# Kernel tuning notes

Hardware: AMD Instinct MI355X
Metric: run time of the kernel (lower is better)

Reference implementation:

```python
import jax, jax.numpy as jnp
import numpy as np

R, M, T = 512, 64, 128
D0, DL, D1, DE = 100, 100, 1000, 100  # embed_dim0, lstm_dim, hidden, embed_dim


def setup_inputs() -> dict:
    key = jax.random.key(0)
    ks = jax.random.split(key, 16)
    s = 0.05
    return {
        "routes": jax.random.normal(ks[0], (R, M, T, 3), dtype=jnp.float32),
        "W0": jax.random.normal(ks[1], (D0, 3), dtype=jnp.float32) * s,
        "b0": jnp.zeros((D0,), dtype=jnp.float32),
        "W_ih": jax.random.normal(ks[2], (4 * DL, D0), dtype=jnp.float32) * s,
        "b_ih": jnp.zeros((4 * DL,), dtype=jnp.float32),
        "W_hh": jax.random.normal(ks[3], (4 * DL, DL), dtype=jnp.float32) * s,
        "b_hh": jnp.zeros((4 * DL,), dtype=jnp.float32),
        "W1": jax.random.normal(ks[4], (D1, DL), dtype=jnp.float32) * s,
        "b1": jnp.zeros((D1,), dtype=jnp.float32),
        "W2": jax.random.normal(ks[5], (DE, D1), dtype=jnp.float32) * s,
        "b2": jnp.zeros((DE,), dtype=jnp.float32),
        "h0": jax.random.uniform(ks[6], (1, DL), dtype=jnp.float32),
        "c0": jax.random.uniform(ks[7], (1, DL), dtype=jnp.float32),
    }


def _forward(routes, W0, b0, W_ih, b_ih, W_hh, b_hh, W1, b1, W2, b2, h0, c0):
    # In the original, LSTMCell is re-run from (h0,c0) at every timestep and hx is
    # overwritten, so only the LAST point of each route matters mathematically.
    last = routes[:, :, -1, :].reshape(-1, 3)           # [R*M, 3]
    x = last @ W0.T + b0                                 # linear0 -> [R*M, D0]
    gates = x @ W_ih.T + b_ih + (h0 @ W_hh.T + b_hh)     # one LSTMCell step, [R*M, 4*DL]
    i, f, g, o = jnp.split(gates, 4, axis=-1)            # PyTorch gate order i,f,g,o
    c = jax.nn.sigmoid(f) * c0 + jax.nn.sigmoid(i) * jnp.tanh(g)
    h = jax.nn.sigmoid(o) * jnp.tanh(c)                  # [R*M, DL]
    h = jax.nn.relu(h @ W1.T + b1) @ W2.T + b2           # MLP -> [R*M, DE]
    emb = h.reshape(R, M, DE).sum(axis=1)                # sum-pool routes -> [R, DE]
    emb = emb / jnp.linalg.norm(emb, axis=-1, keepdims=True)
    cov = emb @ emb.T                                    # cosine similarity [R, R]
    idx = jnp.arange(R)
    return cov.at[idx, idx].set(-jnp.inf)


def reference(routes, W0, b0, W_ih, b_ih, W_hh, b_hh, W1, b1, W2, b2, h0, c0):
    return _forward(routes, W0, b0, W_ih, b_ih, W_hh, b_hh, W1, b1, W2, b2, h0, c0)
```

## Files before the change

kernel.cpp:

```cpp
#include <hip/hip_runtime.h>
#include <hip/hip_bf16.h>
#include <math.h>
#include <float.h>

#define R_ 512
#define M_ 64
#define T_ 128
#define D0_ 100
#define DL_ 100
#define D1_ 1000
#define DE_ 100

#define DIAG_SENTINEL (-1.0e38f)

typedef __attribute__((ext_vector_type(8))) short bf16x8;
typedef __attribute__((ext_vector_type(4))) float f32x4;

__device__ __forceinline__ float sigmoidf_(float x){
  return __builtin_amdgcn_rcpf(1.0f + __expf(-x));
}
__device__ __forceinline__ float tanhf_(float x){
  return 1.0f - 2.0f*__builtin_amdgcn_rcpf(__expf(2.0f*x) + 1.0f);
}
__device__ __forceinline__ short f2bf(float x){
  unsigned u = __builtin_bit_cast(unsigned, x);
  u = (u + 0x7fffu + ((u >> 16) & 1u)) >> 16;
  return (short)u;
}

__global__ __launch_bounds__(256) void k_setup(const float* __restrict__ W1,
                          short* __restrict__ W1pack,
                          const float* __restrict__ W0, const float* __restrict__ b0,
                          const float* __restrict__ W_ih, const float* __restrict__ b_ih,
                          const float* __restrict__ W_hh, const float* __restrict__ b_hh,
                          const float* __restrict__ h0,
                          float* __restrict__ Wc, float* __restrict__ bc) {
  int b = blockIdx.x;
  int tid = threadIdx.x;
  if (b < 64){
    int t = b*256 + tid;
    int l = t & 63, ks = (t>>6)&3, ntile = t>>8;
    int n  = ntile*16 + (l&15);
    int j0 = ks*32 + ((l>>4)<<3);
    bf16x8 v;
    #pragma unroll
    for (int u=0;u<8;++u){
      int j = j0 + u;
      float x = (n < D1_ && j < DL_) ? W1[n*DL_ + j] : 0.f;
      v[u] = f2bf(x);
    }
    ((bf16x8*)W1pack)[t] = v;
  } else {
    int j = (b-64)*256 + tid;
    if (j >= 4*DL_) return;
    float a0=0.f,a1=0.f,a2=0.f,ab=0.f,ah=0.f;
    for (int k=0;k<D0_;++k){
      float w = W_ih[j*D0_+k];
      a0 += w*W0[k*3+0]; a1 += w*W0[k*3+1]; a2 += w*W0[k*3+2];
      ab += w*b0[k];
    }
    for (int k=0;k<DL_;++k) ah += W_hh[j*DL_+k]*h0[k];
    Wc[j*3+0]=a0; Wc[j*3+1]=a1; Wc[j*3+2]=a2;
    bc[j] = ab + b_ih[j] + ah + b_hh[j];
  }
}

__global__ __launch_bounds__(512, 4) void k_fused(const float* __restrict__ routes,
                       const float* __restrict__ Wc, const float* __restrict__ bc,
                       const float* __restrict__ c0,
                       const short* __restrict__ W1pack,
                       const float* __restrict__ b1,
                       const float* __restrict__ W2, const float* __restrict__ b2,
                       float* __restrict__ embT) {
  __shared__ __align__(16) short Hl[8192];
  __shared__ __align__(16) float ts[1000];
  __shared__ float WcS[1200];
  __shared__ float bcS[400];
  __shared__ float c0S[100];
  __shared__ float b1S[1000];
  int r = blockIdx.x;
  int tid = threadIdx.x;
  int w = tid >> 6, l = tid & 63, lr = l & 15;

  float lx[2][3];
  #pragma unroll
  for (int h=0;h<2;++h){
    int mw = h*8 + w;
    int m = mw >> 2;
    int row = r*64 + m*16 + lr;
    const float* lp = routes + ((size_t)row*T_ + (T_-1))*3;
    lx[h][0] = lp[0]; lx[h][1] = lp[1]; lx[h][2] = lp[2];
  }
  for (int i=tid; i<1200; i+=512) WcS[i] = Wc[i];
  for (int i=tid; i<400;  i+=512) bcS[i] = bc[i];
  for (int i=tid; i<100;  i+=512) c0S[i] = c0[i];
  for (int i=tid; i<1000; i+=512) b1S[i] = b1[i];
  __syncthreads();

  {
    int ks = w & 3;
    int j0 = ks*32 + ((l>>4)<<3);
    #pragma unroll
    for (int h=0;h<2;++h){
      int mw = h*8 + w;
      float l0 = lx[h][0], l1 = lx[h][1], l2 = lx[h][2];
      bf16x8 v;
      #pragma unroll
      for (int u=0;u<8;++u){
        int j = j0 + u;
        float hh = 0.f;
        if (j < DL_){
          int ji = j, jf = 100+j, jg = 200+j, jo = 300+j;
          float gi = bcS[ji] + l0*WcS[ji*3+0] + l1*WcS[ji*3+1] + l2*WcS[ji*3+2];
          float gf = bcS[jf] + l0*WcS[jf*3+0] + l1*WcS[jf*3+1] + l2*WcS[jf*3+2];
          float gg = bcS[jg] + l0*WcS[jg*3+0] + l1*WcS[jg*3+1] + l2*WcS[jg*3+2];
          float go = bcS[jo] + l0*WcS[jo*3+0] + l1*WcS[jo*3+1] + l2*WcS[jo*3+2];
          float cc = sigmoidf_(gf)*c0S[j] + sigmoidf_(gi)*tanhf_(gg);
          hh = sigmoidf_(go)*tanhf_(cc);
        }
        v[u] = f2bf(hh);
      }
      *(bf16x8*)&Hl[(mw*64 + l)*8] = v;
    }
  }
  __syncthreads();

  bf16x8 a[4][4];
  #pragma unroll
  for (int m=0;m<4;++m)
    #pragma unroll
    for (int ks=0;ks<4;++ks)
      a[m][ks] = *(const bf16x8*)&Hl[((m*4+ks)*64 + l)*8];

  const bf16x8* Wp = (const bf16x8*)W1pack;
  #pragma unroll 2
  for (int q=0;q<8;++q){
    int ntile = w*8 + q;
    if (ntile == 63) continue;
    f32x4 acc[4];
    #pragma unroll
    for (int m=0;m<4;++m) acc[m] = (f32x4){0.f,0.f,0.f,0.f};
    #pragma unroll
    for (int ks=0;ks<4;++ks){
      bf16x8 bfrag = Wp[(ntile*4+ks)*64 + l];
      #pragma unroll
      for (int m=0;m<4;++m)
        acc[m] = __builtin_amdgcn_mfma_f32_16x16x32_bf16(a[m][ks], bfrag, acc[m], 0, 0, 0);
    }
    int n = ntile*16 + lr;
    float b1n = (n < D1_) ? b1S[n] : 0.f;
    float s = 0.f;
    #pragma unroll
    for (int m=0;m<4;++m){
      #pragma unroll
      for (int jj=0;jj<4;++jj) s += fmaxf(acc[m][jj] + b1n, 0.f);
    }
    s += __shfl_xor(s, 16);
    s += __shfl_xor(s, 32);
    if (l < 16 && n < D1_) ts[n] = s;
  }
  __syncthreads();

  int g = tid >> 2, el = tid & 3;
  if (g < DE_){
    const float4* wrow = (const float4*)(W2 + (size_t)g*D1_);
    const float4* trow = (const float4*)ts;
    float acc = 0.f;
    #pragma unroll 8
    for (int k4 = el; k4 < 250; k4 += 4){
      float4 wv = wrow[k4], tv = trow[k4];
      acc += wv.x*tv.x + wv.y*tv.y + wv.z*tv.z + wv.w*tv.w;
    }
    acc += __shfl_xor(acc, 1);
    acc += __shfl_xor(acc, 2);
    if (el == 0) embT[(size_t)g*R_ + r] = acc + 64.f*b2[g];
  }
}

__global__ __launch_bounds__(256) void k_cov(const float* __restrict__ embT,
                                             float* __restrict__ out) {
  __shared__ float a[2][100];
  int i0 = blockIdx.x * 2, tid = threadIdx.x;
  if (tid < 200){
    int ii = tid & 1, k = tid >> 1;
    a[ii][k] = embT[(size_t)k*R_ + i0 + ii];
  }
  __syncthreads();
  int j = tid, j2 = tid + 256;
  float acc[2] = {0.f,0.f}, acc2[2] = {0.f,0.f};
  float ssi[2] = {0.f,0.f};
  float ssj = 0.f, ssj2 = 0.f;
  #pragma unroll 4
  for (int k=0;k<100;++k){
    float x = embT[(size_t)k*R_ + j];
    float y = embT[(size_t)k*R_ + j2];
    ssj += x*x; ssj2 += y*y;
    #pragma unroll
    for (int ii=0;ii<2;++ii){
      float av = a[ii][k];
      acc[ii]  += av*x;
      acc2[ii] += av*y;
      ssi[ii]  += av*av;
    }
  }
  float rnj  = rsqrtf(ssj);
  float rnj2 = rsqrtf(ssj2);
  #pragma unroll
  for (int ii=0;ii<2;++ii){
    int i = i0 + ii;
    float rni = rsqrtf(ssi[ii]);
    out[(size_t)i*R_ + j]  = (j  == i) ? DIAG_SENTINEL : acc[ii]*rni*rnj;
    out[(size_t)i*R_ + j2] = (j2 == i) ? DIAG_SENTINEL : acc2[ii]*rni*rnj2;
  }
}

extern "C" void kernel_launch(void* const* d_in, const int* in_sizes, int n_in,
                              void* d_out, int out_size, void* d_ws, size_t ws_size,
                              hipStream_t stream) {
  const float* routes = (const float*)d_in[0];
  const float* W0   = (const float*)d_in[1];
  const float* b0   = (const float*)d_in[2];
  const float* W_ih = (const float*)d_in[3];
  const float* b_ih = (const float*)d_in[4];
  const float* W_hh = (const float*)d_in[5];
  const float* b_hh = (const float*)d_in[6];
  const float* W1   = (const float*)d_in[7];
  const float* b1   = (const float*)d_in[8];
  const float* W2   = (const float*)d_in[9];
  const float* b2   = (const float*)d_in[10];
  const float* h0   = (const float*)d_in[11];
  const float* c0   = (const float*)d_in[12];
  float* out = (float*)d_out;

  char* ws = (char*)d_ws;
  short* W1pack = (short*)(ws);
  float* Wc     = (float*)(ws + 262144);
  float* bc     = (float*)(ws + 262144 + 4800);
  float* embT   = (float*)(ws + 268544);

  hipLaunchKernelGGL(k_setup, dim3(66), dim3(256), 0, stream,
                     W1, W1pack, W0,b0,W_ih,b_ih,W_hh,b_hh,h0, Wc, bc);
  hipLaunchKernelGGL(k_fused, dim3(512), dim3(512), 0, stream,
                     routes, Wc, bc, c0, W1pack, b1, W2, b2, embT);
  hipLaunchKernelGGL(k_cov, dim3(256), dim3(256), 0, stream,
                     embT, out);
}
```

Before: 43.05 us.

## Split fused MLP across two blocks per route and batch W2 in separate kernel

The fused kernel now uses two blocks per route, each computing half of the W1 output tiles and writing the pooled hidden sums to global memory. A new k_emb kernel applies W2 for four routes per block, reusing each W2 row across them. The setup kernel's gate-precompute now uses 16 threads per output row with shuffle reductions instead of one serial thread per row. This trades extra global traffic for the intermediate sums and one more kernel launch against more parallelism, higher occupancy, and less per-block serial W2 work.

Result: slower. 104.4 us (+142.4%).

```diff
diff --git a/kernel.cpp b/kernel.cpp
--- a/kernel.cpp
+++ b/kernel.cpp
@@ -51,34 +51,40 @@
     }
     ((bf16x8*)W1pack)[t] = v;
   } else {
-    int j = (b-64)*256 + tid;
-    if (j >= 4*DL_) return;
+    int j = (b-64)*16 + (tid >> 4);
+    int kl = tid & 15;
     float a0=0.f,a1=0.f,a2=0.f,ab=0.f,ah=0.f;
-    for (int k=0;k<D0_;++k){
-      float w = W_ih[j*D0_+k];
+    for (int k = kl; k < D0_; k += 16){
+      float w = W_ih[j*D0_ + k];
       a0 += w*W0[k*3+0]; a1 += w*W0[k*3+1]; a2 += w*W0[k*3+2];
       ab += w*b0[k];
-    }
-    for (int k=0;k<DL_;++k) ah += W_hh[j*DL_+k]*h0[k];
-    Wc[j*3+0]=a0; Wc[j*3+1]=a1; Wc[j*3+2]=a2;
-    bc[j] = ab + b_ih[j] + ah + b_hh[j];
-  }
-}
-
-__global__ __launch_bounds__(512, 4) void k_fused(const float* __restrict__ routes,
+      ah += W_hh[j*DL_ + k]*h0[k];
+    }
+    #pragma unroll
+    for (int m=1;m<16;m<<=1){
+      a0 += __shfl_xor(a0,m); a1 += __shfl_xor(a1,m); a2 += __shfl_xor(a2,m);
+      ab += __shfl_xor(ab,m); ah += __shfl_xor(ah,m);
+    }
+    if (kl == 0){
+      Wc[j*3+0]=a0; Wc[j*3+1]=a1; Wc[j*3+2]=a2;
+      bc[j] = ab + b_ih[j] + ah + b_hh[j];
+    }
+  }
+}
+
+__global__ __launch_bounds__(512, 8) void k_fused(const float* __restrict__ routes,
                        const float* __restrict__ Wc, const float* __restrict__ bc,
                        const float* __restrict__ c0,
                        const short* __restrict__ W1pack,
                        const float* __restrict__ b1,
-                       const float* __restrict__ W2, const float* __restrict__ b2,
-                       float* __restrict__ embT) {
+                       float* __restrict__ tsum) {
   __shared__ __align__(16) short Hl[8192];
-  __shared__ __align__(16) float ts[1000];
   __shared__ float WcS[1200];
   __shared__ float bcS[400];
   __shared__ float c0S[100];
   __shared__ float b1S[1000];
-  int r = blockIdx.x;
+  int r    = blockIdx.x >> 1;
+  int half = blockIdx.x & 1;
   int tid = threadIdx.x;
   int w = tid >> 6, l = tid & 63, lr = l & 15;
 
@@ -134,8 +140,8 @@
 
   const bf16x8* Wp = (const bf16x8*)W1pack;
   #pragma unroll 2
-  for (int q=0;q<8;++q){
-    int ntile = w*8 + q;
+  for (int q=0;q<4;++q){
+    int ntile = half*32 + w*4 + q;
     if (ntile == 63) continue;
     f32x4 acc[4];
     #pragma unroll
@@ -157,23 +163,44 @@
     }
     s += __shfl_xor(s, 16);
     s += __shfl_xor(s, 32);
-    if (l < 16 && n < D1_) ts[n] = s;
-  }
+    if (l < 16 && n < D1_) tsum[(size_t)r*D1_ + n] = s;
+  }
+}
+
+__global__ __launch_bounds__(512) void k_emb(const float* __restrict__ tsum,
+                       const float* __restrict__ W2, const float* __restrict__ b2,
+                       float* __restrict__ embT) {
+  __shared__ __align__(16) float4 tsl[4][250];
+  int r0 = blockIdx.x * 4;
+  int tid = threadIdx.x;
+  const float4* src = (const float4*)(tsum + (size_t)r0*D1_);
+  for (int idx = tid; idx < 1000; idx += 512)
+    ((float4*)tsl)[idx] = src[idx];
   __syncthreads();
 
   int g = tid >> 2, el = tid & 3;
   if (g < DE_){
     const float4* wrow = (const float4*)(W2 + (size_t)g*D1_);
-    const float4* trow = (const float4*)ts;
-    float acc = 0.f;
-    #pragma unroll 8
+    float a0=0.f,a1=0.f,a2=0.f,a3=0.f;
     for (int k4 = el; k4 < 250; k4 += 4){
-      float4 wv = wrow[k4], tv = trow[k4];
-      acc += wv.x*tv.x + wv.y*tv.y + wv.z*tv.z + wv.w*tv.w;
-    }
-    acc += __shfl_xor(acc, 1);
-    acc += __shfl_xor(acc, 2);
-    if (el == 0) embT[(size_t)g*R_ + r] = acc + 64.f*b2[g];
+      float4 wv = wrow[k4];
+      float4 t0 = tsl[0][k4], t1 = tsl[1][k4], t2 = tsl[2][k4], t3 = tsl[3][k4];
+      a0 += wv.x*t0.x + wv.y*t0.y + wv.z*t0.z + wv.w*t0.w;
+      a1 += wv.x*t1.x + wv.y*t1.y + wv.z*t1.z + wv.w*t1.w;
+      a2 += wv.x*t2.x + wv.y*t2.y + wv.z*t2.z + wv.w*t2.w;
+      a3 += wv.x*t3.x + wv.y*t3.y + wv.z*t3.z + wv.w*t3.w;
+    }
+    a0 += __shfl_xor(a0,1); a0 += __shfl_xor(a0,2);
+    a1 += __shfl_xor(a1,1); a1 += __shfl_xor(a1,2);
+    a2 += __shfl_xor(a2,1); a2 += __shfl_xor(a2,2);
+    a3 += __shfl_xor(a3,1); a3 += __shfl_xor(a3,2);
+    if (el == 0){
+      float bb = 64.f*b2[g];
+      embT[(size_t)g*R_ + r0+0] = a0 + bb;
+      embT[(size_t)g*R_ + r0+1] = a1 + bb;
+      embT[(size_t)g*R_ + r0+2] = a2 + bb;
+      embT[(size_t)g*R_ + r0+3] = a3 + bb;
+    }
   }
 }
 
@@ -235,13 +262,16 @@
   char* ws = (char*)d_ws;
   short* W1pack = (short*)(ws);
   float* Wc     = (float*)(ws + 262144);
-  float* bc     = (float*)(ws + 262144 + 4800);
-  float* embT   = (float*)(ws + 268544);
-
-  hipLaunchKernelGGL(k_setup, dim3(66), dim3(256), 0, stream,
+  float* bc     = (float*)(ws + 266944);
+  float* tsum   = (float*)(ws + 268544);
+  float* embT   = (float*)(ws + 2316544);
+
+  hipLaunchKernelGGL(k_setup, dim3(89), dim3(256), 0, stream,
                      W1, W1pack, W0,b0,W_ih,b_ih,W_hh,b_hh,h0, Wc, bc);
-  hipLaunchKernelGGL(k_fused, dim3(512), dim3(512), 0, stream,
-                     routes, Wc, bc, c0, W1pack, b1, W2, b2, embT);
+  hipLaunchKernelGGL(k_fused, dim3(1024), dim3(512), 0, stream,
+                     routes, Wc, bc, c0, W1pack, b1, tsum);
+  hipLaunchKernelGGL(k_emb, dim3(128), dim3(512), 0, stream,
+                     tsum, W2, b2, embT);
   hipLaunchKernelGGL(k_cov, dim3(256), dim3(256), 0, stream,
                      embT, out);
 }
```

## Parallelize gate-weight folding and double fused-kernel threads per route

Applied to the files above, without the earlier changes.

The setup kernel's folding of W0/W_ih/W_hh/h0 into per-gate weights now spreads each output row over 16 lanes with a shuffle reduction. Before, one thread ran two serial 100-step loops per row. The fused kernel now uses 1024 threads per route, so each wave builds one LSTM-output tile and computes 4 W1 n-tiles instead of 8. A fragments are reloaded from LDS inside the MFMA loop instead of being held in 16 registers. This aims to cut serial latency in setup and raise parallelism in the MLP stage, at the cost of extra LDS reads and a tight launch-bounds register budget.

Measured after the change: 41.09 us. 4.6% less time.

```diff
diff --git a/kernel.cpp b/kernel.cpp
--- a/kernel.cpp
+++ b/kernel.cpp
@@ -51,21 +51,28 @@
     }
     ((bf16x8*)W1pack)[t] = v;
   } else {
-    int j = (b-64)*256 + tid;
-    if (j >= 4*DL_) return;
+    int j = (b-64)*16 + (tid >> 4);
+    int kl = tid & 15;
     float a0=0.f,a1=0.f,a2=0.f,ab=0.f,ah=0.f;
-    for (int k=0;k<D0_;++k){
-      float w = W_ih[j*D0_+k];
+    for (int k = kl; k < D0_; k += 16){
+      float w = W_ih[j*D0_ + k];
       a0 += w*W0[k*3+0]; a1 += w*W0[k*3+1]; a2 += w*W0[k*3+2];
       ab += w*b0[k];
-    }
-    for (int k=0;k<DL_;++k) ah += W_hh[j*DL_+k]*h0[k];
-    Wc[j*3+0]=a0; Wc[j*3+1]=a1; Wc[j*3+2]=a2;
-    bc[j] = ab + b_ih[j] + ah + b_hh[j];
-  }
-}
-
-__global__ __launch_bounds__(512, 4) void k_fused(const float* __restrict__ routes,
+      ah += W_hh[j*DL_ + k]*h0[k];
+    }
+    #pragma unroll
+    for (int m=1;m<16;m<<=1){
+      a0 += __shfl_xor(a0,m); a1 += __shfl_xor(a1,m); a2 += __shfl_xor(a2,m);
+      ab += __shfl_xor(ab,m); ah += __shfl_xor(ah,m);
+    }
+    if (kl == 0){
+      Wc[j*3+0]=a0; Wc[j*3+1]=a1; Wc[j*3+2]=a2;
+      bc[j] = ab + b_ih[j] + ah + b_hh[j];
+    }
+  }
+}
+
+__global__ __launch_bounds__(1024, 8) void k_fused(const float* __restrict__ routes,
                        const float* __restrict__ Wc, const float* __restrict__ bc,
                        const float* __restrict__ c0,
                        const short* __restrict__ W1pack,
@@ -82,60 +89,45 @@
   int tid = threadIdx.x;
   int w = tid >> 6, l = tid & 63, lr = l & 15;
 
-  float lx[2][3];
-  #pragma unroll
-  for (int h=0;h<2;++h){
-    int mw = h*8 + w;
-    int m = mw >> 2;
-    int row = r*64 + m*16 + lr;
-    const float* lp = routes + ((size_t)row*T_ + (T_-1))*3;
-    lx[h][0] = lp[0]; lx[h][1] = lp[1]; lx[h][2] = lp[2];
-  }
-  for (int i=tid; i<1200; i+=512) WcS[i] = Wc[i];
-  for (int i=tid; i<400;  i+=512) bcS[i] = bc[i];
-  for (int i=tid; i<100;  i+=512) c0S[i] = c0[i];
-  for (int i=tid; i<1000; i+=512) b1S[i] = b1[i];
+  int m_  = w >> 2;
+  int ks_ = w & 3;
+  int row = r*64 + m_*16 + lr;
+
+  const float* lp = routes + ((size_t)row*T_ + (T_-1))*3;
+  float l0 = lp[0], l1 = lp[1], l2 = lp[2];
+
+  for (int i=tid; i<1200; i+=1024) WcS[i] = Wc[i];
+  if (tid < 400) bcS[tid] = bc[tid];
+  if (tid < 100) c0S[tid] = c0[tid];
+  if (tid < 1000) b1S[tid] = b1[tid];
   __syncthreads();
 
   {
-    int ks = w & 3;
-    int j0 = ks*32 + ((l>>4)<<3);
-    #pragma unroll
-    for (int h=0;h<2;++h){
-      int mw = h*8 + w;
-      float l0 = lx[h][0], l1 = lx[h][1], l2 = lx[h][2];
-      bf16x8 v;
-      #pragma unroll
-      for (int u=0;u<8;++u){
-        int j = j0 + u;
-        float hh = 0.f;
-        if (j < DL_){
-          int ji = j, jf = 100+j, jg = 200+j, jo = 300+j;
-          float gi = bcS[ji] + l0*WcS[ji*3+0] + l1*WcS[ji*3+1] + l2*WcS[ji*3+2];
-          float gf = bcS[jf] + l0*WcS[jf*3+0] + l1*WcS[jf*3+1] + l2*WcS[jf*3+2];
-          float gg = bcS[jg] + l0*WcS[jg*3+0] + l1*WcS[jg*3+1] + l2*WcS[jg*3+2];
-          float go = bcS[jo] + l0*WcS[jo*3+0] + l1*WcS[jo*3+1] + l2*WcS[jo*3+2];
-          float cc = sigmoidf_(gf)*c0S[j] + sigmoidf_(gi)*tanhf_(gg);
-          hh = sigmoidf_(go)*tanhf_(cc);
-        }
-        v[u] = f2bf(hh);
+    int j0 = ks_*32 + ((l>>4)<<3);
+    bf16x8 v;
+    #pragma unroll
+    for (int u=0;u<8;++u){
+      int j = j0 + u;
+      float hh = 0.f;
+      if (j < DL_){
+        int ji = j, jf = 100+j, jg = 200+j, jo = 300+j;
+        float gi = bcS[ji] + l0*WcS[ji*3+0] + l1*WcS[ji*3+1] + l2*WcS[ji*3+2];
+        float gf = bcS[jf] + l0*WcS[jf*3+0] + l1*WcS[jf*3+1] + l2*WcS[jf*3+2];
+        float gg = bcS[jg] + l0*WcS[jg*3+0] + l1*WcS[jg*3+1] + l2*WcS[jg*3+2];
+        float go = bcS[jo] + l0*WcS[jo*3+0] + l1*WcS[jo*3+1] + l2*WcS[jo*3+2];
+        float cc = sigmoidf_(gf)*c0S[j] + sigmoidf_(gi)*tanhf_(gg);
+        hh = sigmoidf_(go)*tanhf_(cc);
       }
-      *(bf16x8*)&Hl[(mw*64 + l)*8] = v;
-    }
-  }
-  __syncthreads();
-
-  bf16x8 a[4][4];
-  #pragma unroll
-  for (int m=0;m<4;++m)
-    #pragma unroll
-    for (int ks=0;ks<4;++ks)
-      a[m][ks] = *(const bf16x8*)&Hl[((m*4+ks)*64 + l)*8];
+      v[u] = f2bf(hh);
+    }
+    *(bf16x8*)&Hl[(w*64 + l)*8] = v;
+  }
+  __syncthreads();
 
   const bf16x8* Wp = (const bf16x8*)W1pack;
-  #pragma unroll 2
-  for (int q=0;q<8;++q){
-    int ntile = w*8 + q;
+  #pragma unroll 1
+  for (int q=0;q<4;++q){
+    int ntile = w*4 + q;
     if (ntile == 63) continue;
     f32x4 acc[4];
     #pragma unroll
@@ -143,9 +135,14 @@
     #pragma unroll
     for (int ks=0;ks<4;++ks){
       bf16x8 bfrag = Wp[(ntile*4+ks)*64 + l];
-      #pragma unroll
-      for (int m=0;m<4;++m)
-        acc[m] = __builtin_amdgcn_mfma_f32_16x16x32_bf16(a[m][ks], bfrag, acc[m], 0, 0, 0);
+      bf16x8 a0 = *(const bf16x8*)&Hl[((0*4+ks)*64 + l)*8];
+      bf16x8 a1 = *(const bf16x8*)&Hl[((1*4+ks)*64 + l)*8];
+      bf16x8 a2 = *(const bf16x8*)&Hl[((2*4+ks)*64 + l)*8];
+      bf16x8 a3 = *(const bf16x8*)&Hl[((3*4+ks)*64 + l)*8];
+      acc[0] = __builtin_amdgcn_mfma_f32_16x16x32_bf16(a0, bfrag, acc[0], 0, 0, 0);
+      acc[1] = __builtin_amdgcn_mfma_f32_16x16x32_bf16(a1, bfrag, acc[1], 0, 0, 0);
+      acc[2] = __builtin_amdgcn_mfma_f32_16x16x32_bf16(a2, bfrag, acc[2], 0, 0, 0);
+      acc[3] = __builtin_amdgcn_mfma_f32_16x16x32_bf16(a3, bfrag, acc[3], 0, 0, 0);
     }
     int n = ntile*16 + lr;
     float b1n = (n < D1_) ? b1S[n] : 0.f;
@@ -235,12 +232,12 @@
   char* ws = (char*)d_ws;
   short* W1pack = (short*)(ws);
   float* Wc     = (float*)(ws + 262144);
-  float* bc     = (float*)(ws + 262144 + 4800);
+  float* bc     = (float*)(ws + 266944);
   float* embT   = (float*)(ws + 268544);
 
-  hipLaunchKernelGGL(k_setup, dim3(66), dim3(256), 0, stream,
+  hipLaunchKernelGGL(k_setup, dim3(89), dim3(256), 0, stream,
                      W1, W1pack, W0,b0,W_ih,b_ih,W_hh,b_hh,h0, Wc, bc);
-  hipLaunchKernelGGL(k_fused, dim3(512), dim3(512), 0, stream,
+  hipLaunchKernelGGL(k_fused, dim3(512), dim3(1024), 0, stream,
                      routes, Wc, bc, c0, W1pack, b1, W2, b2, embT);
   hipLaunchKernelGGL(k_cov, dim3(256), dim3(256), 0, stream,
                      embT, out);
```
